# Kernel tuning notes

Hardware: AMD Instinct MI355X
Metric: run time of the kernel (lower is better)

## Reference

```python
import jax, jax.numpy as jnp
from jax import lax
import numpy as np

B, T = 256, 512
CHAR_SIZE, CHAR_DIM, HIDDEN = 10000, 50, 256
HALF = HIDDEN // 2  # per-direction hidden size


def _lstm_dir(x, Wih, Whh, bih, bhh, reverse):
    # x: [B,T,D]; Wih: [4H,D]; Whh: [4H,H]; gate order i,f,g,o (PyTorch)
    Bsz = x.shape[0]
    H = Whh.shape[1]
    xg = jnp.einsum('btd,gd->btg', x, Wih) + bih + bhh  # precompute input gates [B,T,4H]
    def step(carry, gt):
        h, c = carry
        g = gt + h @ Whh.T
        i, f, gg, o = jnp.split(g, 4, axis=-1)
        c = jax.nn.sigmoid(f) * c + jax.nn.sigmoid(i) * jnp.tanh(gg)
        h = jax.nn.sigmoid(o) * jnp.tanh(c)
        return (h, c), h
    init = (jnp.zeros((Bsz, H), x.dtype), jnp.zeros((Bsz, H), x.dtype))
    _, hs = lax.scan(step, init, jnp.swapaxes(xg, 0, 1), reverse=reverse)
    return jnp.swapaxes(hs, 0, 1)  # [B,T,H]


def setup_inputs() -> dict:
    key = jax.random.key(0)
    ks = jax.random.split(key, 10)
    scale = np.sqrt(3.0 / CHAR_DIM)
    inp = {
        'user_text_idx': jax.random.randint(ks[0], (B, T), 0, CHAR_SIZE),
        'masks': jnp.ones((B, T), jnp.float32),
        'emb': jax.random.uniform(ks[1], (CHAR_SIZE, CHAR_DIM), jnp.float32, -scale, scale),
        'Wih_f': jax.random.normal(ks[2], (4 * HALF, CHAR_DIM), jnp.float32) * 0.08,
        'Whh_f': jax.random.normal(ks[3], (4 * HALF, HALF), jnp.float32) * 0.08,
        'bih_f': jnp.zeros((4 * HALF,), jnp.float32),
        'bhh_f': jnp.zeros((4 * HALF,), jnp.float32),
        'Wih_b': jax.random.normal(ks[4], (4 * HALF, CHAR_DIM), jnp.float32) * 0.08,
        'Whh_b': jax.random.normal(ks[5], (4 * HALF, HALF), jnp.float32) * 0.08,
        'bih_b': jnp.zeros((4 * HALF,), jnp.float32),
        'bhh_b': jnp.zeros((4 * HALF,), jnp.float32),
    }
    return inp


def reference(user_text_idx, masks, emb, Wih_f, Whh_f, bih_f, bhh_f, Wih_b, Whh_b, bih_b, bhh_b):
    x = emb[user_text_idx]                                  # [B,T,D] embedding lookup
    h_f = _lstm_dir(x, Wih_f, Whh_f, bih_f, bhh_f, False)   # forward direction
    h_b = _lstm_dir(x, Wih_b, Whh_b, bih_b, bhh_b, True)    # backward direction
    out = jnp.concatenate([h_f, h_b], axis=-1)              # [B,T,HIDDEN]
    out = out - (1.0 - masks[..., None]) * 1e8              # mask pad positions
    return jnp.max(out, axis=-2)                            # masked max-pool -> [B,HIDDEN]
```

## Files before the change

### kernel.cpp

```cpp
#include <hip/hip_runtime.h>
#include <hip/hip_fp16.h>


#define TT 512
#define CH 2

typedef _Float16 f16;
typedef _Float16 f16x8 __attribute__((ext_vector_type(8)));
typedef float f32x4 __attribute__((ext_vector_type(4)));
typedef unsigned int u32;
typedef unsigned short u16;

static __device__ __forceinline__ u32 packh2(float lo, float hi) {
    union { struct { f16 x, y; } h; u32 u; } cv;
    cv.h.x = (f16)lo; cv.h.y = (f16)hi;
    return cv.u;
}
static __device__ __forceinline__ float fexp(float x) {
    return __builtin_amdgcn_exp2f(x * 1.44269504088896341f);
}
static __device__ __forceinline__ float frcp(float x) {
    return __builtin_amdgcn_rcpf(x);
}
static __device__ __forceinline__ float sigf(float x) {
    return frcp(1.f + fexp(-x));
}
static __device__ __forceinline__ float xor8(float x) {
    union { float f; int i; } c; c.f = x;
    c.i = __builtin_amdgcn_mov_dpp(c.i, 0x128, 0xF, 0xF, false);
    return c.f;
}
static __device__ __forceinline__ float xor2(float x) {
    union { float f; int i; } c; c.f = x;
    c.i = __builtin_amdgcn_mov_dpp(c.i, 0x4E, 0xF, 0xF, false);
    return c.f;
}
static __device__ __forceinline__ float sel4(f32x4 v, int q) {
    return (q & 2) ? ((q & 1) ? v[3] : v[2]) : ((q & 1) ? v[1] : v[0]);
}

__global__ __attribute__((amdgpu_flat_work_group_size(512, 512),
                          amdgpu_waves_per_eu(2, 2)))
void bilstm_compact_kernel(const int* __restrict__ idx,
                           const float* __restrict__ masks,
                           const float* __restrict__ emb,
                           const float* __restrict__ Wih_f, const float* __restrict__ Whh_f,
                           const float* __restrict__ bih_f, const float* __restrict__ bhh_f,
                           const float* __restrict__ Wih_b, const float* __restrict__ Whh_b,
                           const float* __restrict__ bih_b, const float* __restrict__ bhh_b,
                           float* __restrict__ out)
{
    __shared__ __align__(16) u16 Hc[2][CH][192];
    __shared__ u16 idx16[CH * TT];
    __shared__ u32 mbits[TT];

    const int tid  = threadIdx.x;
    const int lane = tid & 63;
    const int wv   = tid >> 6;
    const int l15  = lane & 15;
    const int c4   = lane >> 4;
    const int d    = blockIdx.x & 1;
    const int g    = blockIdx.x >> 1;
    const int b0   = g * CH;
    const int rev  = d;

    const int chain = l15 & 1;
    const int q     = (l15 >> 1) & 3;
    const int role  = l15 >> 3;

    const float* Wih = d ? Wih_b : Wih_f;
    const float* Whh = d ? Whh_b : Whh_f;
    const float* bih = d ? bih_b : bih_f;
    const float* bhh = d ? bhh_b : bhh_f;

    for (int i = tid; i < CH * TT; i += 512) {
        const int m = i >> 9, t = i & 511;
        idx16[i] = (u16)idx[(b0 + m) * TT + t];
    }
    if (tid < TT) {
        u32 mb = 0;
        for (int m = 0; m < CH; ++m)
            mb |= (masks[(b0 + m) * TT + tid] != 0.f ? 1u : 0u) << m;
        mbits[tid] = mb;
    }
    if (tid < 2 * CH * 192 / 2) {
        ((u32*)Hc)[tid] = 0u;
    }

    f16x8 w[6][4];
    f32x4 bias4[4];
#pragma unroll
    for (int gt = 0; gt < 4; ++gt) {
        const int n = (wv + gt * 8) * 16 + l15;
        {
            const int nb_ = (wv + gt * 8) * 16 + c4 * 4;
            const float4 bi = *(const float4*)(bih + nb_);
            const float4 bh = *(const float4*)(bhh + nb_);
            bias4[gt][0] = bi.x + bh.x; bias4[gt][1] = bi.y + bh.y;
            bias4[gt][2] = bi.z + bh.z; bias4[gt][3] = bi.w + bh.w;
        }
#pragma unroll
        for (int jj = 0; jj < 4; ++jj) {
            const float2 e = *(const float2*)(Wih + n * 50 + c4 * 8 + jj * 2);
            w[0][gt][2 * jj]     = (f16)e.x;
            w[0][gt][2 * jj + 1] = (f16)e.y;
        }
#pragma unroll
        for (int j = 0; j < 8; ++j) {
            const int k = 32 + c4 * 8 + j;
            float v = 0.f;
            if (k < 50) v = Wih[n * 50 + k];
            w[1][gt][j] = (f16)v;
        }
#pragma unroll
        for (int kt = 2; kt < 6; ++kt) {
            const int kh = (kt - 2) * 32 + c4 * 8;
            const float4 e0 = *(const float4*)(Whh + n * 128 + kh);
            const float4 e1 = *(const float4*)(Whh + n * 128 + kh + 4);
            w[kt][gt][0] = (f16)e0.x; w[kt][gt][1] = (f16)e0.y;
            w[kt][gt][2] = (f16)e0.z; w[kt][gt][3] = (f16)e0.w;
            w[kt][gt][4] = (f16)e1.x; w[kt][gt][5] = (f16)e1.y;
            w[kt][gt][6] = (f16)e1.z; w[kt][gt][7] = (f16)e1.w;
        }
    }

    __syncthreads();

    const int  tid7 = tid - 448;
    const bool xthr = (tid7 >= 0) && (tid7 < 50);
    const int  xch  = xthr ? (tid7 / 25) : 0;
    const int  xps  = xthr ? (tid7 % 25) : 0;

    if (xthr) {
        const int t0  = rev ? (TT - 1) : 0;
        const int row = idx16[xch * TT + t0];
        const float2 e = *(const float2*)(emb + row * 50 + xps * 2);
        *(u32*)((unsigned char*)&Hc[0][0][0] + xch * 384 + xps * 4) =
            packh2(e.x, e.y);
    }
    __syncthreads();

    float cst = 0.f, rm = -3e38f;

    const int hd = wv * 16 + c4 * 4 + q;
    const bool wbthr = (l15 == 0) | (l15 == 1) | (l15 == 4) | (l15 == 5);

    for (int s = 0; s < TT; ++s) {
        const int cur = s & 1;
        const int t   = rev ? (TT - 1 - s) : s;

        float2 e;
        const bool pf = xthr && (s + 1 < TT);
        if (pf) {
            const int t1  = rev ? (TT - 2 - s) : (s + 1);
            const int row = idx16[xch * TT + t1];
            e = *(const float2*)(emb + row * 50 + xps * 2);
        }

        const unsigned char* hb =
            (const unsigned char*)&Hc[cur][0][0] + chain * 384;
        f32x4 ai = bias4[0], af = bias4[1], ag = bias4[2], ao = bias4[3];
#pragma unroll
        for (int kt = 0; kt < 6; ++kt) {
            const f16x8 bf = *(const f16x8*)(hb + kt * 64 + c4 * 16);
            ai = __builtin_amdgcn_mfma_f32_16x16x32_f16(w[kt][0], bf, ai, 0, 0, 0);
            af = __builtin_amdgcn_mfma_f32_16x16x32_f16(w[kt][1], bf, af, 0, 0, 0);
            ag = __builtin_amdgcn_mfma_f32_16x16x32_f16(w[kt][2], bf, ag, 0, 0, 0);
            ao = __builtin_amdgcn_mfma_f32_16x16x32_f16(w[kt][3], bf, ao, 0, 0, 0);
        }

        const float iv = sel4(ai, q);
        const float fv = sel4(af, q);
        const float gv = sel4(ag, q);
        const float ov = sel4(ao, q);

        const bool rB = (role != 0);
        const float u_in = rB ? (gv + gv) : fv;
        const float v_in = rB ? ov : iv;
        const float su = sigf(u_in);
        const float sv = sigf(v_in);
        const float tg_send = 2.f * su - 1.f;
        const float tgx = xor8(tg_send);
        const float svx = xor8(sv);
        const float cc = su * cst + sv * tgx;
        cst = cc;
        const float ccx = xor8(cc);
        const float cc_use = rB ? ccx : cc;
        const float th = 2.f * sigf(cc_use + cc_use) - 1.f;
        const float so_use = rB ? sv : svx;
        const float hh = so_use * th;

        const float pen = ((mbits[t] >> chain) & 1u) ? 0.f : 1e8f;
        rm = fmaxf(rm, hh - pen);

        unsigned char* nb = (unsigned char*)&Hc[cur ^ 1][0][0];
        const float hx2 = xor2(hh);
        if (wbthr) {
            *(u32*)(nb + chain * 384 + 128 + hd * 2) = packh2(hh, hx2);
        }
        if (pf) {
            *(u32*)(nb + xch * 384 + xps * 4) = packh2(e.x, e.y);
        }
        __syncthreads();
    }

    if (l15 < 8) {
        out[(b0 + chain) * 256 + d * 128 + hd] = rm;
    }
}

extern "C" void kernel_launch(void* const* d_in, const int* in_sizes, int n_in,
                              void* d_out, int out_size, void* d_ws, size_t ws_size,
                              hipStream_t stream) {
    const int*   idx   = (const int*)d_in[0];
    const float* masks = (const float*)d_in[1];
    const float* emb   = (const float*)d_in[2];
    const float* Wih_f = (const float*)d_in[3];
    const float* Whh_f = (const float*)d_in[4];
    const float* bih_f = (const float*)d_in[5];
    const float* bhh_f = (const float*)d_in[6];
    const float* Wih_b = (const float*)d_in[7];
    const float* Whh_b = (const float*)d_in[8];
    const float* bih_b = (const float*)d_in[9];
    const float* bhh_b = (const float*)d_in[10];
    float* out = (float*)d_out;

    bilstm_compact_kernel<<<dim3(256), dim3(512), 0, stream>>>(
        idx, masks, emb,
        Wih_f, Whh_f, bih_f, bhh_f,
        Wih_b, Whh_b, bih_b, bhh_b,
        out);
}
```

Baseline: 381.4 us.

## Run both directions of one sequence per 1024-thread block, fold bias into MFMA

Each block now handles a single batch row, with both LSTM directions in one 1024-thread block, split into 8 waves per direction. Before, each 512-thread block handled two batch rows in one direction. The bias is folded into the input weight matrix through a constant-one column at k=50, so the accumulators start at zero and the per-block bias registers go away. The lane mapping changes so each 16-lane group now serves one chain, and hidden-state write-back uses a xor1 DPP swap. The cost is a larger block with a per-step __syncthreads across 16 waves, a 128-VGPR cap, and one lane group doing roughly half-redundant work per MFMA column.

```diff
diff --git a/kernel.cpp b/kernel.cpp
--- a/kernel.cpp
+++ b/kernel.cpp
@@ -3,7 +3,6 @@
 
 
 #define TT 512
-#define CH 2
 
 typedef _Float16 f16;
 typedef _Float16 f16x8 __attribute__((ext_vector_type(8)));
@@ -30,75 +29,61 @@
     c.i = __builtin_amdgcn_mov_dpp(c.i, 0x128, 0xF, 0xF, false);
     return c.f;
 }
-static __device__ __forceinline__ float xor2(float x) {
+static __device__ __forceinline__ float xor1(float x) {
     union { float f; int i; } c; c.f = x;
-    c.i = __builtin_amdgcn_mov_dpp(c.i, 0x4E, 0xF, 0xF, false);
+    c.i = __builtin_amdgcn_mov_dpp(c.i, 0xB1, 0xF, 0xF, false);
     return c.f;
 }
 static __device__ __forceinline__ float sel4(f32x4 v, int q) {
     return (q & 2) ? ((q & 1) ? v[3] : v[2]) : ((q & 1) ? v[1] : v[0]);
 }
 
-__global__ __attribute__((amdgpu_flat_work_group_size(512, 512),
-                          amdgpu_waves_per_eu(2, 2)))
-void bilstm_compact_kernel(const int* __restrict__ idx,
-                           const float* __restrict__ masks,
-                           const float* __restrict__ emb,
-                           const float* __restrict__ Wih_f, const float* __restrict__ Whh_f,
-                           const float* __restrict__ bih_f, const float* __restrict__ bhh_f,
-                           const float* __restrict__ Wih_b, const float* __restrict__ Whh_b,
-                           const float* __restrict__ bih_b, const float* __restrict__ bhh_b,
-                           float* __restrict__ out)
+__global__ __attribute__((amdgpu_flat_work_group_size(1024, 1024),
+                          amdgpu_num_vgpr(128)))
+void bilstm_dual_kernel(const int* __restrict__ idx,
+                        const float* __restrict__ masks,
+                        const float* __restrict__ emb,
+                        const float* __restrict__ Wih_f, const float* __restrict__ Whh_f,
+                        const float* __restrict__ bih_f, const float* __restrict__ bhh_f,
+                        const float* __restrict__ Wih_b, const float* __restrict__ Whh_b,
+                        const float* __restrict__ bih_b, const float* __restrict__ bhh_b,
+                        float* __restrict__ out)
 {
-    __shared__ __align__(16) u16 Hc[2][CH][192];
-    __shared__ u16 idx16[CH * TT];
+    __shared__ __align__(16) u16 Hc[2][2][192];
+    __shared__ u16 idx16[TT];
     __shared__ u32 mbits[TT];
 
     const int tid  = threadIdx.x;
     const int lane = tid & 63;
     const int wv   = tid >> 6;
+    const int half = wv >> 3;
+    const int wvh  = wv & 7;
     const int l15  = lane & 15;
     const int c4   = lane >> 4;
-    const int d    = blockIdx.x & 1;
-    const int g    = blockIdx.x >> 1;
-    const int b0   = g * CH;
-    const int rev  = d;
-
-    const int chain = l15 & 1;
-    const int q     = (l15 >> 1) & 3;
-    const int role  = l15 >> 3;
-
-    const float* Wih = d ? Wih_b : Wih_f;
-    const float* Whh = d ? Whh_b : Whh_f;
-    const float* bih = d ? bih_b : bih_f;
-    const float* bhh = d ? bhh_b : bhh_f;
-
-    for (int i = tid; i < CH * TT; i += 512) {
-        const int m = i >> 9, t = i & 511;
-        idx16[i] = (u16)idx[(b0 + m) * TT + t];
-    }
+    const int b0   = blockIdx.x;
+    const int rev  = half;
+
+    const int q  = l15 & 3;
+    const bool rB = (l15 >> 3) != 0;
+
+    const float* Wih = half ? Wih_b : Wih_f;
+    const float* Whh = half ? Whh_b : Whh_f;
+    const float* bih = half ? bih_b : bih_f;
+    const float* bhh = half ? bhh_b : bhh_f;
+
     if (tid < TT) {
-        u32 mb = 0;
-        for (int m = 0; m < CH; ++m)
-            mb |= (masks[(b0 + m) * TT + tid] != 0.f ? 1u : 0u) << m;
-        mbits[tid] = mb;
-    }
-    if (tid < 2 * CH * 192 / 2) {
-        ((u32*)Hc)[tid] = 0u;
+        idx16[tid] = (u16)idx[b0 * TT + tid];
+        mbits[tid] = (masks[b0 * TT + tid] != 0.f) ? 1u : 0u;
+    }
+    if (tid < 384) {
+        const int kpair = (tid % 96) * 2;
+        ((u32*)Hc)[tid] = (kpair == 50) ? 0x00003C00u : 0u;
     }
 
     f16x8 w[6][4];
-    f32x4 bias4[4];
 #pragma unroll
     for (int gt = 0; gt < 4; ++gt) {
-        const int n = (wv + gt * 8) * 16 + l15;
-        {
-            const int nb_ = (wv + gt * 8) * 16 + c4 * 4;
-            const float4 bi = *(const float4*)(bih + nb_);
-            const float4 bh = *(const float4*)(bhh + nb_);
-            bias4[gt][0] = bi.x + bh.x; bias4[gt][1] = bi.y + bh.y;
-            bias4[gt][2] = bi.z + bh.z; bias4[gt][3] = bi.w + bh.w;
-        }
+        const int n = (wvh + gt * 8) * 16 + l15;
 #pragma unroll
         for (int jj = 0; jj < 4; ++jj) {
             const float2 e = *(const float2*)(Wih + n * 50 + c4 * 8 + jj * 2);
@@ -109,7 +94,8 @@
         for (int j = 0; j < 8; ++j) {
             const int k = 32 + c4 * 8 + j;
             float v = 0.f;
-            if (k < 50) v = Wih[n * 50 + k];
+            if (k < 50)       v = Wih[n * 50 + k];
+            else if (k == 50) v = bih[n] + bhh[n];
             w[1][gt][j] = (f16)v;
         }
 #pragma unroll
@@ -126,24 +112,18 @@
 
     __syncthreads();
 
-    const int  tid7 = tid - 448;
-    const bool xthr = (tid7 >= 0) && (tid7 < 50);
-    const int  xch  = xthr ? (tid7 / 25) : 0;
-    const int  xps  = xthr ? (tid7 % 25) : 0;
+    const bool xthr = (wvh == 7) && (lane < 25);
 
     if (xthr) {
         const int t0  = rev ? (TT - 1) : 0;
-        const int row = idx16[xch * TT + t0];
-        const float2 e = *(const float2*)(emb + row * 50 + xps * 2);
-        *(u32*)((unsigned char*)&Hc[0][0][0] + xch * 384 + xps * 4) =
-            packh2(e.x, e.y);
+        const int row = idx16[t0];
+        const float2 e = *(const float2*)(emb + row * 50 + lane * 2);
+        *(u32*)((unsigned char*)&Hc[0][half][0] + lane * 4) = packh2(e.x, e.y);
     }
     __syncthreads();
 
     float cst = 0.f, rm = -3e38f;
-
-    const int hd = wv * 16 + c4 * 4 + q;
-    const bool wbthr = (l15 == 0) | (l15 == 1) | (l15 == 4) | (l15 == 5);
+    const int hd = wvh * 16 + c4 * 4 + q;
 
     for (int s = 0; s < TT; ++s) {
         const int cur = s & 1;
@@ -153,13 +133,13 @@
         const bool pf = xthr && (s + 1 < TT);
         if (pf) {
             const int t1  = rev ? (TT - 2 - s) : (s + 1);
-            const int row = idx16[xch * TT + t1];
-            e = *(const float2*)(emb + row * 50 + xps * 2);
-        }
-
-        const unsigned char* hb =
-            (const unsigned char*)&Hc[cur][0][0] + chain * 384;
-        f32x4 ai = bias4[0], af = bias4[1], ag = bias4[2], ao = bias4[3];
+            const int row = idx16[t1];
+            e = *(const float2*)(emb + row * 50 + lane * 2);
+        }
+
+        const unsigned char* hb = (const unsigned char*)&Hc[cur][half][0];
+        const f32x4 z = {0.f, 0.f, 0.f, 0.f};
+        f32x4 ai = z, af = z, ag = z, ao = z;
 #pragma unroll
         for (int kt = 0; kt < 6; ++kt) {
             const f16x8 bf = *(const f16x8*)(hb + kt * 64 + c4 * 16);
@@ -174,7 +154,6 @@
         const float gv = sel4(ag, q);
         const float ov = sel4(ao, q);
 
-        const bool rB = (role != 0);
         const float u_in = rB ? (gv + gv) : fv;
         const float v_in = rB ? ov : iv;
         const float su = sigf(u_in);
@@ -190,22 +169,22 @@
         const float so_use = rB ? sv : svx;
         const float hh = so_use * th;
 
-        const float pen = ((mbits[t] >> chain) & 1u) ? 0.f : 1e8f;
+        const float pen = mbits[t] ? 0.f : 1e8f;
         rm = fmaxf(rm, hh - pen);
 
-        unsigned char* nb = (unsigned char*)&Hc[cur ^ 1][0][0];
-        const float hx2 = xor2(hh);
-        if (wbthr) {
-            *(u32*)(nb + chain * 384 + 128 + hd * 2) = packh2(hh, hx2);
+        unsigned char* nb = (unsigned char*)&Hc[cur ^ 1][half][0];
+        const float hx = xor1(hh);
+        if (l15 == 0 || l15 == 2) {
+            *(u32*)(nb + 128 + hd * 2) = packh2(hh, hx);
         }
         if (pf) {
-            *(u32*)(nb + xch * 384 + xps * 4) = packh2(e.x, e.y);
+            *(u32*)(nb + lane * 4) = packh2(e.x, e.y);
         }
         __syncthreads();
     }
 
-    if (l15 < 8) {
-        out[(b0 + chain) * 256 + d * 128 + hd] = rm;
+    if (l15 < 4) {
+        out[b0 * 256 + half * 128 + hd] = rm;
     }
 }
 
@@ -225,7 +204,7 @@
     const float* bhh_b = (const float*)d_in[10];
     float* out = (float*)d_out;
 
-    bilstm_compact_kernel<<<dim3(256), dim3(512), 0, stream>>>(
+    bilstm_dual_kernel<<<dim3(256), dim3(1024), 0, stream>>>(
         idx, masks, emb,
         Wih_f, Whh_f, bih_f, bhh_f,
         Wih_b, Whh_b, bih_b, bhh_b,
```

Result: slower. 754.8 us (+97.9%).

## Precompute per-vocabulary input-gate projections into workspace table

Applied to the files above, without the earlier changes.

Adds a pre-pass kernel that computes Wih·emb[v] plus biases for every vocabulary row and both directions, storing the results as fp16 in the workspace. The recurrent kernel then gathers these precomputed gate inputs per timestep instead of running input-projection MFMAs, which drops the per-step MFMA count from 24 to 16 and removes the embedding staging in shared memory. The cost is an extra launch and a 20 MB table build over the whole vocabulary, plus fp16 rounding of the input gates. The path is used only when the workspace is large enough, otherwise it falls back to the old kernel.

```diff
diff --git a/kernel.cpp b/kernel.cpp
--- a/kernel.cpp
+++ b/kernel.cpp
@@ -4,6 +4,7 @@
 
 #define TT 512
 #define CH 2
+#define XE_U16 (2 * 10000 * 512)
 
 typedef _Float16 f16;
 typedef _Float16 f16x8 __attribute__((ext_vector_type(8)));
@@ -16,6 +17,9 @@
     cv.h.x = (f16)lo; cv.h.y = (f16)hi;
     return cv.u;
 }
+static __device__ __forceinline__ u16 f16bits(float v) {
+    union { f16 h; u16 u; } cv; cv.h = (f16)v; return cv.u;
+}
 static __device__ __forceinline__ float fexp(float x) {
     return __builtin_amdgcn_exp2f(x * 1.44269504088896341f);
 }
@@ -37,6 +41,195 @@
 }
 static __device__ __forceinline__ float sel4(f32x4 v, int q) {
     return (q & 2) ? ((q & 1) ? v[3] : v[2]) : ((q & 1) ? v[1] : v[0]);
+}
+static __device__ __forceinline__ f32x4 cvt4(uint2 u) {
+    union { uint2 u2; f16 h[4]; } cv; cv.u2 = u;
+    f32x4 r;
+    r[0] = (float)cv.h[0]; r[1] = (float)cv.h[1];
+    r[2] = (float)cv.h[2]; r[3] = (float)cv.h[3];
+    return r;
+}
+
+__global__ __launch_bounds__(128)
+void xe_precompute_kernel(const float* __restrict__ emb,
+                          const float* __restrict__ Wih_f,
+                          const float* __restrict__ bih_f, const float* __restrict__ bhh_f,
+                          const float* __restrict__ Wih_b,
+                          const float* __restrict__ bih_b, const float* __restrict__ bhh_b,
+                          u16* __restrict__ xe)
+{
+    const int v    = blockIdx.x % 10000;
+    const int ddir = blockIdx.x / 10000;
+    const float* Wih = ddir ? Wih_b : Wih_f;
+    const float* bih = ddir ? bih_b : bih_f;
+    const float* bhh = ddir ? bhh_b : bhh_f;
+
+    __shared__ float xrow[50];
+    const int tid = threadIdx.x;
+    if (tid < 50) xrow[tid] = emb[v * 50 + tid];
+    __syncthreads();
+
+    const int wv = tid >> 4, gt = (tid >> 2) & 3, c4 = tid & 3;
+    const int g0 = (wv + gt * 8) * 16 + c4 * 4;
+
+    float a[4];
+#pragma unroll
+    for (int q = 0; q < 4; ++q) {
+        const float* wr = Wih + (g0 + q) * 50;
+        float acc = bih[g0 + q] + bhh[g0 + q];
+#pragma unroll
+        for (int kk = 0; kk < 25; ++kk) {
+            const float2 w2 = *(const float2*)(wr + kk * 2);
+            acc += xrow[2 * kk] * w2.x + xrow[2 * kk + 1] * w2.y;
+        }
+        a[q] = acc;
+    }
+    u16* dst = xe + (ddir * 10000 + v) * 512 + tid * 4;
+    dst[0] = f16bits(a[0]); dst[1] = f16bits(a[1]);
+    dst[2] = f16bits(a[2]); dst[3] = f16bits(a[3]);
+}
+
+__global__ __launch_bounds__(512)
+void bilstm_xe_kernel(const int* __restrict__ idx,
+                      const float* __restrict__ masks,
+                      const u16* __restrict__ xe,
+                      const float* __restrict__ Whh_f,
+                      const float* __restrict__ Whh_b,
+                      float* __restrict__ out)
+{
+    __shared__ __align__(16) u16 Hc[2][CH][128];
+    __shared__ u16 idx16[CH * TT];
+    __shared__ u32 mbits[TT];
+
+    const int tid  = threadIdx.x;
+    const int lane = tid & 63;
+    const int wv   = tid >> 6;
+    const int l15  = lane & 15;
+    const int c4   = lane >> 4;
+    const int d    = blockIdx.x & 1;
+    const int g    = blockIdx.x >> 1;
+    const int b0   = g * CH;
+    const int rev  = d;
+
+    const int chain = l15 & 1;
+    const int q     = (l15 >> 1) & 3;
+    const bool rB   = (l15 >> 3) != 0;
+
+    const float* Whh = d ? Whh_b : Whh_f;
+
+    for (int i = tid; i < CH * TT; i += 512) {
+        const int m = i >> 9, t = i & 511;
+        idx16[i] = (u16)idx[(b0 + m) * TT + t];
+    }
+    if (tid < TT) {
+        u32 mb = 0;
+        for (int m = 0; m < CH; ++m)
+            mb |= (masks[(b0 + m) * TT + tid] != 0.f ? 1u : 0u) << m;
+        mbits[tid] = mb;
+    }
+    if (tid < 2 * CH * 128 / 2) {
+        ((u32*)Hc)[tid] = 0u;
+    }
+
+    f16x8 w[4][4];
+#pragma unroll
+    for (int gt = 0; gt < 4; ++gt) {
+        const int n = (wv + gt * 8) * 16 + l15;
+#pragma unroll
+        for (int kt = 0; kt < 4; ++kt) {
+            const int kh = kt * 32 + c4 * 8;
+            const float4 e0 = *(const float4*)(Whh + n * 128 + kh);
+            const float4 e1 = *(const float4*)(Whh + n * 128 + kh + 4);
+            w[kt][gt][0] = (f16)e0.x; w[kt][gt][1] = (f16)e0.y;
+            w[kt][gt][2] = (f16)e0.z; w[kt][gt][3] = (f16)e0.w;
+            w[kt][gt][4] = (f16)e1.x; w[kt][gt][5] = (f16)e1.y;
+            w[kt][gt][6] = (f16)e1.z; w[kt][gt][7] = (f16)e1.w;
+        }
+    }
+
+    __syncthreads();
+
+    const int ubase = (wv * 16 + c4) * 4;
+    const int xrowmul = 512;
+    const int xdbase = d * 10000 * 512;
+
+    uint2 xw0, xw1, xw2, xw3;
+    {
+        const int t0  = rev ? (TT - 1) : 0;
+        const int row = idx16[chain * TT + t0];
+        const u16* rb = xe + xdbase + row * xrowmul + ubase;
+        xw0 = *(const uint2*)(rb);
+        xw1 = *(const uint2*)(rb + 16);
+        xw2 = *(const uint2*)(rb + 32);
+        xw3 = *(const uint2*)(rb + 48);
+    }
+
+    float cst = 0.f, rm = -3e38f;
+    const int hd = wv * 16 + c4 * 4 + q;
+    const bool wbthr = (l15 == 0) | (l15 == 1) | (l15 == 4) | (l15 == 5);
+
+    for (int s = 0; s < TT; ++s) {
+        const int cur = s & 1;
+        const int t   = rev ? (TT - 1 - s) : s;
+
+        f32x4 ai = cvt4(xw0), af = cvt4(xw1), ag = cvt4(xw2), ao = cvt4(xw3);
+
+        const bool pf = (s + 1 < TT);
+        if (pf) {
+            const int t1  = rev ? (TT - 2 - s) : (s + 1);
+            const int row = idx16[chain * TT + t1];
+            const u16* rb = xe + xdbase + row * xrowmul + ubase;
+            xw0 = *(const uint2*)(rb);
+            xw1 = *(const uint2*)(rb + 16);
+            xw2 = *(const uint2*)(rb + 32);
+            xw3 = *(const uint2*)(rb + 48);
+        }
+
+        const unsigned char* hb =
+            (const unsigned char*)&Hc[cur][0][0] + chain * 256;
+#pragma unroll
+        for (int kt = 0; kt < 4; ++kt) {
+            const f16x8 bf = *(const f16x8*)(hb + kt * 64 + c4 * 16);
+            ai = __builtin_amdgcn_mfma_f32_16x16x32_f16(w[kt][0], bf, ai, 0, 0, 0);
+            af = __builtin_amdgcn_mfma_f32_16x16x32_f16(w[kt][1], bf, af, 0, 0, 0);
+            ag = __builtin_amdgcn_mfma_f32_16x16x32_f16(w[kt][2], bf, ag, 0, 0, 0);
+            ao = __builtin_amdgcn_mfma_f32_16x16x32_f16(w[kt][3], bf, ao, 0, 0, 0);
+        }
+
+        const float iv = sel4(ai, q);
+        const float fv = sel4(af, q);
+        const float gv = sel4(ag, q);
+        const float ov = sel4(ao, q);
+
+        const float u_in = rB ? (gv + gv) : fv;
+        const float v_in = rB ? ov : iv;
+        const float su = sigf(u_in);
+        const float sv = sigf(v_in);
+        const float tg_send = 2.f * su - 1.f;
+        const float tgx = xor8(tg_send);
+        const float svx = xor8(sv);
+        const float cc = su * cst + sv * tgx;
+        cst = cc;
+        const float ccx = xor8(cc);
+        const float cc_use = rB ? ccx : cc;
+        const float th = 2.f * sigf(cc_use + cc_use) - 1.f;
+        const float so_use = rB ? sv : svx;
+        const float hh = so_use * th;
+
+        const float pen = ((mbits[t] >> chain) & 1u) ? 0.f : 1e8f;
+        rm = fmaxf(rm, hh - pen);
+
+        unsigned char* nb = (unsigned char*)&Hc[cur ^ 1][0][0];
+        const float hx2 = xor2(hh);
+        if (wbthr) {
+            *(u32*)(nb + chain * 256 + hd * 2) = packh2(hh, hx2);
+        }
+        __syncthreads();
+    }
+
+    if (l15 < 8) {
+        out[(b0 + chain) * 256 + d * 128 + hd] = rm;
+    }
 }
 
 __global__ __attribute__((amdgpu_flat_work_group_size(512, 512),
@@ -63,7 +256,6 @@
     const int g    = blockIdx.x >> 1;
     const int b0   = g * CH;
     const int rev  = d;
-
     const int chain = l15 & 1;
     const int q     = (l15 >> 1) & 3;
     const int role  = l15 >> 3;
@@ -83,9 +275,7 @@
             mb |= (masks[(b0 + m) * TT + tid] != 0.f ? 1u : 0u) << m;
         mbits[tid] = mb;
     }
-    if (tid < 2 * CH * 192 / 2) {
-        ((u32*)Hc)[tid] = 0u;
-    }
+    if (tid < 2 * CH * 192 / 2) ((u32*)Hc)[tid] = 0u;
 
     f16x8 w[6][4];
     f32x4 bias4[4];
@@ -123,14 +313,12 @@
             w[kt][gt][6] = (f16)e1.z; w[kt][gt][7] = (f16)e1.w;
         }
     }
-
     __syncthreads();
 
     const int  tid7 = tid - 448;
     const bool xthr = (tid7 >= 0) && (tid7 < 50);
     const int  xch  = xthr ? (tid7 / 25) : 0;
     const int  xps  = xthr ? (tid7 % 25) : 0;
-
     if (xthr) {
         const int t0  = rev ? (TT - 1) : 0;
         const int row = idx16[xch * TT + t0];
@@ -141,14 +329,12 @@
     __syncthreads();
 
     float cst = 0.f, rm = -3e38f;
-
     const int hd = wv * 16 + c4 * 4 + q;
     const bool wbthr = (l15 == 0) | (l15 == 1) | (l15 == 4) | (l15 == 5);
 
     for (int s = 0; s < TT; ++s) {
         const int cur = s & 1;
         const int t   = rev ? (TT - 1 - s) : s;
-
         float2 e;
         const bool pf = xthr && (s + 1 < TT);
         if (pf) {
@@ -156,7 +342,6 @@
             const int row = idx16[xch * TT + t1];
             e = *(const float2*)(emb + row * 50 + xps * 2);
         }
-
         const unsigned char* hb =
             (const unsigned char*)&Hc[cur][0][0] + chain * 384;
         f32x4 ai = bias4[0], af = bias4[1], ag = bias4[2], ao = bias4[3];
@@ -168,12 +353,10 @@
             ag = __builtin_amdgcn_mfma_f32_16x16x32_f16(w[kt][2], bf, ag, 0, 0, 0);
             ao = __builtin_amdgcn_mfma_f32_16x16x32_f16(w[kt][3], bf, ao, 0, 0, 0);
         }
-
         const float iv = sel4(ai, q);
         const float fv = sel4(af, q);
         const float gv = sel4(ag, q);
         const float ov = sel4(ao, q);
-
         const bool rB = (role != 0);
         const float u_in = rB ? (gv + gv) : fv;
         const float v_in = rB ? ov : iv;
@@ -189,10 +372,8 @@
         const float th = 2.f * sigf(cc_use + cc_use) - 1.f;
         const float so_use = rB ? sv : svx;
         const float hh = so_use * th;
-
         const float pen = ((mbits[t] >> chain) & 1u) ? 0.f : 1e8f;
         rm = fmaxf(rm, hh - pen);
-
         unsigned char* nb = (unsigned char*)&Hc[cur ^ 1][0][0];
         const float hx2 = xor2(hh);
         if (wbthr) {
@@ -203,7 +384,6 @@
         }
         __syncthreads();
     }
-
     if (l15 < 8) {
         out[(b0 + chain) * 256 + d * 128 + hd] = rm;
     }
@@ -225,9 +405,18 @@
     const float* bhh_b = (const float*)d_in[10];
     float* out = (float*)d_out;
 
-    bilstm_compact_kernel<<<dim3(256), dim3(512), 0, stream>>>(
-        idx, masks, emb,
-        Wih_f, Whh_f, bih_f, bhh_f,
-        Wih_b, Whh_b, bih_b, bhh_b,
-        out);
-}
+    const size_t xe_bytes = (size_t)XE_U16 * sizeof(u16);
+    if (ws_size >= xe_bytes) {
+        u16* xe = (u16*)d_ws;
+        xe_precompute_kernel<<<dim3(20000), dim3(128), 0, stream>>>(
+            emb, Wih_f, bih_f, bhh_f, Wih_b, bih_b, bhh_b, xe);
+        bilstm_xe_kernel<<<dim3(256), dim3(512), 0, stream>>>(
+            idx, masks, xe, Whh_f, Whh_b, out);
+    } else {
+        bilstm_compact_kernel<<<dim3(256), dim3(512), 0, stream>>>(
+            idx, masks, emb,
+            Wih_f, Whh_f, bih_f, bhh_f,
+            Wih_b, Whh_b, bih_b, bhh_b,
+            out);
+    }
+}
```

After: 724.9 us. +90.0%, slower.

## Precompute next step's input-gate MFMAs off the recurrent critical path

Applied to the files above, without the earlier changes.

Splits the input projection out of the per-step recurrent matmul. The x contribution for step s+1 is computed during step s, using a triple-buffered embedding staging area filled two steps ahead. The dependent chain per step shrinks from 6 to 4 K-tiles of MFMA, and the 8 x MFMAs can overlap with the gate nonlinearities. The cost is extra registers for the x accumulators and a longer prefetch distance.

```diff
diff --git a/kernel.cpp b/kernel.cpp
--- a/kernel.cpp
+++ b/kernel.cpp
@@ -41,16 +41,17 @@
 
 __global__ __attribute__((amdgpu_flat_work_group_size(512, 512),
                           amdgpu_waves_per_eu(2, 2)))
-void bilstm_compact_kernel(const int* __restrict__ idx,
-                           const float* __restrict__ masks,
-                           const float* __restrict__ emb,
-                           const float* __restrict__ Wih_f, const float* __restrict__ Whh_f,
-                           const float* __restrict__ bih_f, const float* __restrict__ bhh_f,
-                           const float* __restrict__ Wih_b, const float* __restrict__ Whh_b,
-                           const float* __restrict__ bih_b, const float* __restrict__ bhh_b,
-                           float* __restrict__ out)
+void bilstm_xla_kernel(const int* __restrict__ idx,
+                       const float* __restrict__ masks,
+                       const float* __restrict__ emb,
+                       const float* __restrict__ Wih_f, const float* __restrict__ Whh_f,
+                       const float* __restrict__ bih_f, const float* __restrict__ bhh_f,
+                       const float* __restrict__ Wih_b, const float* __restrict__ Whh_b,
+                       const float* __restrict__ bih_b, const float* __restrict__ bhh_b,
+                       float* __restrict__ out)
 {
-    __shared__ __align__(16) u16 Hc[2][CH][192];
+    __shared__ __align__(16) u16 Hc[2][CH][128];
+    __shared__ __align__(16) u16 Xb[3][CH][64];
     __shared__ u16 idx16[CH * TT];
     __shared__ u32 mbits[TT];
 
@@ -83,9 +84,8 @@
             mb |= (masks[(b0 + m) * TT + tid] != 0.f ? 1u : 0u) << m;
         mbits[tid] = mb;
     }
-    if (tid < 2 * CH * 192 / 2) {
-        ((u32*)Hc)[tid] = 0u;
-    }
+    if (tid < 256) ((u32*)Hc)[tid] = 0u;
+    if (tid < 192) ((u32*)Xb)[tid] = 0u;
 
     f16x8 w[6][4];
     f32x4 bias4[4];
@@ -132,41 +132,78 @@
     const int  xps  = xthr ? (tid7 % 25) : 0;
 
     if (xthr) {
-        const int t0  = rev ? (TT - 1) : 0;
-        const int row = idx16[xch * TT + t0];
-        const float2 e = *(const float2*)(emb + row * 50 + xps * 2);
-        *(u32*)((unsigned char*)&Hc[0][0][0] + xch * 384 + xps * 4) =
-            packh2(e.x, e.y);
+#pragma unroll
+        for (int p = 0; p < 2; ++p) {
+            const int tp  = rev ? (TT - 1 - p) : p;
+            const int row = idx16[xch * TT + tp];
+            const float2 e = *(const float2*)(emb + row * 50 + xps * 2);
+            *(u32*)((unsigned char*)&Xb[p][0][0] + xch * 128 + xps * 4) =
+                packh2(e.x, e.y);
+        }
     }
     __syncthreads();
+
+    f32x4 xi = bias4[0], xf = bias4[1], xg = bias4[2], xo = bias4[3];
+    {
+        const unsigned char* xb =
+            (const unsigned char*)&Xb[0][0][0] + chain * 128;
+        const f16x8 b0 = *(const f16x8*)(xb + c4 * 16);
+        const f16x8 b1 = *(const f16x8*)(xb + 64 + c4 * 16);
+        xi = __builtin_amdgcn_mfma_f32_16x16x32_f16(w[0][0], b0, xi, 0, 0, 0);
+        xf = __builtin_amdgcn_mfma_f32_16x16x32_f16(w[0][1], b0, xf, 0, 0, 0);
+        xg = __builtin_amdgcn_mfma_f32_16x16x32_f16(w[0][2], b0, xg, 0, 0, 0);
+        xo = __builtin_amdgcn_mfma_f32_16x16x32_f16(w[0][3], b0, xo, 0, 0, 0);
+        xi = __builtin_amdgcn_mfma_f32_16x16x32_f16(w[1][0], b1, xi, 0, 0, 0);
+        xf = __builtin_amdgcn_mfma_f32_16x16x32_f16(w[1][1], b1, xf, 0, 0, 0);
+        xg = __builtin_amdgcn_mfma_f32_16x16x32_f16(w[1][2], b1, xg, 0, 0, 0);
+        xo = __builtin_amdgcn_mfma_f32_16x16x32_f16(w[1][3], b1, xo, 0, 0, 0);
+    }
 
     float cst = 0.f, rm = -3e38f;
 
     const int hd = wv * 16 + c4 * 4 + q;
     const bool wbthr = (l15 == 0) | (l15 == 1) | (l15 == 4) | (l15 == 5);
+
+    int p1 = 1, p2 = 2, p0 = 0;
 
     for (int s = 0; s < TT; ++s) {
         const int cur = s & 1;
         const int t   = rev ? (TT - 1 - s) : s;
 
         float2 e;
-        const bool pf = xthr && (s + 1 < TT);
+        const bool pf = xthr && (s + 2 < TT);
         if (pf) {
-            const int t1  = rev ? (TT - 2 - s) : (s + 1);
-            const int row = idx16[xch * TT + t1];
+            const int t2  = rev ? (TT - 3 - s) : (s + 2);
+            const int row = idx16[xch * TT + t2];
             e = *(const float2*)(emb + row * 50 + xps * 2);
         }
 
         const unsigned char* hb =
-            (const unsigned char*)&Hc[cur][0][0] + chain * 384;
-        f32x4 ai = bias4[0], af = bias4[1], ag = bias4[2], ao = bias4[3];
-#pragma unroll
-        for (int kt = 0; kt < 6; ++kt) {
+            (const unsigned char*)&Hc[cur][0][0] + chain * 256;
+        f32x4 ai = xi, af = xf, ag = xg, ao = xo;
+#pragma unroll
+        for (int kt = 0; kt < 4; ++kt) {
             const f16x8 bf = *(const f16x8*)(hb + kt * 64 + c4 * 16);
-            ai = __builtin_amdgcn_mfma_f32_16x16x32_f16(w[kt][0], bf, ai, 0, 0, 0);
-            af = __builtin_amdgcn_mfma_f32_16x16x32_f16(w[kt][1], bf, af, 0, 0, 0);
-            ag = __builtin_amdgcn_mfma_f32_16x16x32_f16(w[kt][2], bf, ag, 0, 0, 0);
-            ao = __builtin_amdgcn_mfma_f32_16x16x32_f16(w[kt][3], bf, ao, 0, 0, 0);
+            ai = __builtin_amdgcn_mfma_f32_16x16x32_f16(w[kt + 2][0], bf, ai, 0, 0, 0);
+            af = __builtin_amdgcn_mfma_f32_16x16x32_f16(w[kt + 2][1], bf, af, 0, 0, 0);
+            ag = __builtin_amdgcn_mfma_f32_16x16x32_f16(w[kt + 2][2], bf, ag, 0, 0, 0);
+            ao = __builtin_amdgcn_mfma_f32_16x16x32_f16(w[kt + 2][3], bf, ao, 0, 0, 0);
+        }
+
+        xi = bias4[0]; xf = bias4[1]; xg = bias4[2]; xo = bias4[3];
+        {
+            const unsigned char* xb =
+                (const unsigned char*)&Xb[0][0][0] + p1 * 256 + chain * 128;
+            const f16x8 b0 = *(const f16x8*)(xb + c4 * 16);
+            const f16x8 b1 = *(const f16x8*)(xb + 64 + c4 * 16);
+            xi = __builtin_amdgcn_mfma_f32_16x16x32_f16(w[0][0], b0, xi, 0, 0, 0);
+            xf = __builtin_amdgcn_mfma_f32_16x16x32_f16(w[0][1], b0, xf, 0, 0, 0);
+            xg = __builtin_amdgcn_mfma_f32_16x16x32_f16(w[0][2], b0, xg, 0, 0, 0);
+            xo = __builtin_amdgcn_mfma_f32_16x16x32_f16(w[0][3], b0, xo, 0, 0, 0);
+            xi = __builtin_amdgcn_mfma_f32_16x16x32_f16(w[1][0], b1, xi, 0, 0, 0);
+            xf = __builtin_amdgcn_mfma_f32_16x16x32_f16(w[1][1], b1, xf, 0, 0, 0);
+            xg = __builtin_amdgcn_mfma_f32_16x16x32_f16(w[1][2], b1, xg, 0, 0, 0);
+            xo = __builtin_amdgcn_mfma_f32_16x16x32_f16(w[1][3], b1, xo, 0, 0, 0);
         }
 
         const float iv = sel4(ai, q);
@@ -193,15 +230,18 @@
         const float pen = ((mbits[t] >> chain) & 1u) ? 0.f : 1e8f;
         rm = fmaxf(rm, hh - pen);
 
-        unsigned char* nb = (unsigned char*)&Hc[cur ^ 1][0][0];
         const float hx2 = xor2(hh);
         if (wbthr) {
-            *(u32*)(nb + chain * 384 + 128 + hd * 2) = packh2(hh, hx2);
+            *(u32*)((unsigned char*)&Hc[cur ^ 1][0][0] + chain * 256 + hd * 2) =
+                packh2(hh, hx2);
         }
         if (pf) {
-            *(u32*)(nb + xch * 384 + xps * 4) = packh2(e.x, e.y);
+            *(u32*)((unsigned char*)&Xb[0][0][0] + p2 * 256 + xch * 128 + xps * 4) =
+                packh2(e.x, e.y);
         }
         __syncthreads();
+
+        const int tmp = p0; p0 = p1; p1 = p2; p2 = tmp;
     }
 
     if (l15 < 8) {
@@ -225,7 +265,7 @@
     const float* bhh_b = (const float*)d_in[10];
     float* out = (float*)d_out;
 
-    bilstm_compact_kernel<<<dim3(256), dim3(512), 0, stream>>>(
+    bilstm_xla_kernel<<<dim3(256), dim3(512), 0, stream>>>(
         idx, masks, emb,
         Wih_f, Whh_f, bih_f, bhh_f,
         Wih_b, Whh_b, bih_b, bhh_b,
```

After: 374.0 us. About the same (-1.9%).
